# Kernel optimization log

Hardware: AMD Instinct MI355X
Metric: run time of the kernel (lower is better)

## Reference

```python
import jax, jax.numpy as jnp
import numpy as np

EPS = 1e-8  # torch F.cosine_similarity eps

B, H, K = 64, 2048, 256


def setup_inputs() -> dict:
    key = jax.random.key(0)
    k1, k2, k3, k4 = jax.random.split(key, 4)
    input_state = jax.random.normal(k1, (B, H), dtype=jnp.float32)
    knowledge_base = jax.random.normal(k2, (K, B, H), dtype=jnp.float32)
    W = jax.random.normal(k3, (H, H), dtype=jnp.float32) / np.sqrt(H)
    b = jax.random.normal(k4, (H,), dtype=jnp.float32) * 0.02
    return {"input_state": input_state, "knowledge_base": knowledge_base, "W": W, "b": b}


def reference(input_state, knowledge_base, W, b):
    # linear projection (torch Linear: x @ W.T + b)
    q = input_state @ W.T + b                      # [B, H]
    kproj = jnp.einsum('kbh,oh->kbo', knowledge_base, W) + b  # [K, B, H]
    # cosine similarity over last dim, with torch-style eps clamp on norms
    qn = jnp.maximum(jnp.linalg.norm(q, axis=-1), EPS)        # [B]
    kn = jnp.maximum(jnp.linalg.norm(kproj, axis=-1), EPS)    # [K, B]
    dots = jnp.einsum('bh,kbh->kb', q, kproj)                 # [K, B]
    scores = dots / (qn[None, :] * kn)                        # [K, B]
    # softmax over the K knowledge items
    attn = jax.nn.softmax(scores, axis=0)                     # [K, B]
    # output = input + softmax-weighted sum of (raw) knowledge items
    out = input_state + jnp.einsum('kb,kbh->bh', attn, knowledge_base)
    return out
```

## Files before the change

### kernel.cpp

```cpp
#include <hip/hip_runtime.h>
#include <hip/hip_bf16.h>

typedef unsigned short u16;
typedef unsigned int u32;
typedef unsigned long long u64;
typedef __attribute__((ext_vector_type(8))) short short8;
typedef __attribute__((ext_vector_type(4))) float float4v;

#define B_DIM 64
#define H_DIM 2048
#define K_DIM 256
#define NTHR  256

#define WS_WBF   0ull
#define WS_AQ    (8388608ull)
#define WS_Q     (WS_AQ + 524288ull)
#define WS_KN2   (WS_Q + 524288ull)
#define WS_DOTS  (WS_KN2 + 65536ull)
#define WS_KBF   (WS_DOTS + 65536ull)

__device__ __forceinline__ u16 f2bf(float f) {
    unsigned int u = __float_as_uint(f);
    unsigned int r = (u + 0x7fffu + ((u >> 16) & 1u)) >> 16;
    return (u16)r;
}

__device__ __forceinline__ u64 pack4(float4v v) {
    u64 a0 = f2bf(v.x), a1 = f2bf(v.y), a2 = f2bf(v.z), a3 = f2bf(v.w);
    return a0 | (a1 << 16) | (a2 << 32) | (a3 << 48);
}

__device__ __forceinline__ void llds16(const u16* g, u16* l) {
    __builtin_amdgcn_global_load_lds(
        (__attribute__((address_space(1))) void*)g,
        (__attribute__((address_space(3))) void*)l, 16, 0, 0);
}

__device__ __forceinline__ void gemm0_tile(const u16* __restrict__ Aq, const u16* __restrict__ Wb,
                                           float* __restrict__ qout, u16* As, u16* Bs,
                                           int nt, int ksplit) {
    const int tid = threadIdx.x;
    const int wave = tid >> 6, lane = tid & 63;
    const int l15 = lane & 15, qd = lane >> 4;
    const int wm = wave >> 1, wn = wave & 1;
    const int n0 = nt * 128;
    const int grow = lane >> 2;
    const int gcol = (((lane & 3) ^ ((lane >> 3) & 3)) * 8);
    const int sw = (l15 >> 1) & 3;
    float4v acc[4][4] = {};
    const int kb0 = ksplit * 512;
    for (int kk = 0; kk < 16; ++kk) {
        const int k0 = kb0 + kk * 32;
        #pragma unroll
        for (int i = 0; i < 2; ++i) {
            const int r = wave * 32 + i * 16;
            llds16(Wb + (size_t)(n0 + r + grow) * H_DIM + k0 + gcol, &Bs[r * 32]);
            llds16(Aq + (size_t)(r + grow) * H_DIM + k0 + gcol, &As[r * 32]);
        }
        __syncthreads();
        short8 af[4], bf_[4];
        #pragma unroll
        for (int mi = 0; mi < 4; ++mi)
            af[mi] = *(const short8*)&As[(wm * 64 + mi * 16 + l15) * 32 + ((qd ^ sw) * 8)];
        #pragma unroll
        for (int ni = 0; ni < 4; ++ni)
            bf_[ni] = *(const short8*)&Bs[(wn * 64 + ni * 16 + l15) * 32 + ((qd ^ sw) * 8)];
        #pragma unroll
        for (int mi = 0; mi < 4; ++mi)
            #pragma unroll
            for (int ni = 0; ni < 4; ++ni)
                acc[mi][ni] = __builtin_amdgcn_mfma_f32_16x16x32_bf16(af[mi], bf_[ni], acc[mi][ni], 0, 0, 0);
        __syncthreads();
    }
    const int n0w = n0 + wn * 64;
    if (wm == 0) {
        #pragma unroll
        for (int mi = 0; mi < 4; ++mi)
            #pragma unroll
            for (int reg = 0; reg < 4; ++reg) {
                const int m = mi * 16 + qd * 4 + reg;
                #pragma unroll
                for (int ni = 0; ni < 4; ++ni)
                    atomicAdd(&qout[m * H_DIM + n0w + ni * 16 + l15], acc[mi][ni][reg]);
            }
    }
}

__global__ __launch_bounds__(256) void prep_kernel(
        const float* __restrict__ W, const float* __restrict__ input,
        const float* __restrict__ bias, u16* __restrict__ Wb,
        u16* __restrict__ Aq, float* __restrict__ q,
        float* __restrict__ kn2, float* __restrict__ dots) {
    const int gid = blockIdx.x * NTHR + threadIdx.x;
    ((u64*)Wb)[gid] = pack4(((const float4v*)W)[gid]);
    if (gid < 65536) {
        u64 v = 0;
        if (gid < 32768) v = pack4(((const float4v*)input)[gid]);
        ((u64*)Aq)[gid] = v;
    }
    if (gid < 32768)
        ((float4v*)q)[gid] = ((const float4v*)bias)[gid & 511];
    if (gid < 4096) ((float4v*)kn2)[gid] = float4v{0.f, 0.f, 0.f, 0.f};
    else if (gid < 8192) ((float4v*)dots)[gid - 4096] = float4v{0.f, 0.f, 0.f, 0.f};
}

__global__ __launch_bounds__(256, 4) void mid_kernel(
        const float* __restrict__ kb, const u16* __restrict__ Aq,
        const u16* __restrict__ Wb, float* __restrict__ q, u16* __restrict__ Kbf) {
    __shared__ __align__(16) u16 As[128 * 32];
    __shared__ __align__(16) u16 Bs[128 * 32];
    const int bid = blockIdx.x;
    if (bid < 64) {
        gemm0_tile(Aq, Wb, q, As, Bs, bid & 15, bid >> 4);
    } else {
        const float4v* s4 = (const float4v*)kb;
        u64* d8 = (u64*)Kbf;
        for (int i = (bid - 64) * NTHR + threadIdx.x; i < 8388608; i += 960 * NTHR)
            d8[i] = pack4(s4[i]);
    }
}

__global__ __launch_bounds__(512, 2) void gemm_kernel(
        const u16* __restrict__ Kbf, const u16* __restrict__ Wb,
        const float* __restrict__ bias, const float* __restrict__ q,
        float* __restrict__ kn2, float* __restrict__ dots) {
    extern __shared__ __align__(16) u16 lds[];
    const int tid = threadIdx.x;
    const int wave = tid >> 6, lane = tid & 63;
    const int l15 = lane & 15, qd = lane >> 4;
    const int wm = wave >> 2, wn = wave & 3;
    const int nt = blockIdx.x & 7, mt = blockIdx.x >> 3;
    const int m0 = mt * 256, n0 = nt * 256;
    const int grow = wave * 16 + (lane >> 2);
    const int gcol = (((lane & 3) ^ ((lane >> 3) & 3)) * 8);
    const int sw = (l15 >> 1) & 3;

    const u16* srcA = Kbf + (size_t)(m0 + grow) * H_DIM + gcol;
    const u16* srcB = Wb + (size_t)(n0 + grow) * H_DIM + gcol;
    u16* dstBase = lds + wave * 512;

    auto stageA = [&](int t) {
        u16* d = dstBase + (t & 3) * 16384;
        const u16* s = srcA + t * 32;
        llds16(s, d);
        llds16(s + (size_t)128 * H_DIM, d + 4096);
    };
    auto stageB = [&](int t) {
        u16* d = dstBase + (t & 3) * 16384 + 8192;
        const u16* s = srcB + t * 32;
        llds16(s, d);
        llds16(s + (size_t)128 * H_DIM, d + 4096);
    };

    const int aoff = (wm * 128 + l15) * 32 + ((qd ^ sw) * 8);
    const int boff = (wn * 64 + l15) * 32 + ((qd ^ sw) * 8);

    float4v acc[8][4] = {};

    stageA(0); stageB(0); stageA(1); stageB(1); stageA(2); stageB(2);
    asm volatile("s_waitcnt vmcnt(8)" ::: "memory");
    __builtin_amdgcn_sched_barrier(0);
    __builtin_amdgcn_s_barrier();

    for (int t = 0; t < 64; ++t) {
        const u16* As = lds + (t & 3) * 16384;
        const u16* Bs = As + 8192;
        short8 af[4], bf_[4];
        #pragma unroll
        for (int ni = 0; ni < 4; ++ni)
            bf_[ni] = *(const short8*)&Bs[boff + ni * 512];
        #pragma unroll
        for (int mi = 0; mi < 4; ++mi)
            af[mi] = *(const short8*)&As[aoff + mi * 512];
        if (t + 3 < 64) stageA(t + 3);
        __builtin_amdgcn_s_barrier();
        asm volatile("s_waitcnt lgkmcnt(0)" ::: "memory");
        __builtin_amdgcn_sched_barrier(0);
        __builtin_amdgcn_s_setprio(1);
        #pragma unroll
        for (int mi = 0; mi < 4; ++mi)
            #pragma unroll
            for (int ni = 0; ni < 4; ++ni)
                acc[mi][ni] = __builtin_amdgcn_mfma_f32_16x16x32_bf16(af[mi], bf_[ni], acc[mi][ni], 0, 0, 0);
        __builtin_amdgcn_s_setprio(0);
        __builtin_amdgcn_s_barrier();
        #pragma unroll
        for (int mi = 0; mi < 4; ++mi)
            af[mi] = *(const short8*)&As[aoff + (4 + mi) * 512];
        if (t + 3 < 64) stageB(t + 3);
        __builtin_amdgcn_s_barrier();
        asm volatile("s_waitcnt lgkmcnt(0)" ::: "memory");
        __builtin_amdgcn_sched_barrier(0);
        __builtin_amdgcn_s_setprio(1);
        #pragma unroll
        for (int mi = 0; mi < 4; ++mi)
            #pragma unroll
            for (int ni = 0; ni < 4; ++ni)
                acc[4 + mi][ni] = __builtin_amdgcn_mfma_f32_16x16x32_bf16(af[mi], bf_[ni], acc[4 + mi][ni], 0, 0, 0);
        __builtin_amdgcn_s_setprio(0);
        if (t <= 60)      { asm volatile("s_waitcnt vmcnt(8)" ::: "memory"); }
        else if (t == 61) { asm volatile("s_waitcnt vmcnt(4)" ::: "memory"); }
        else if (t == 62) { asm volatile("s_waitcnt vmcnt(0)" ::: "memory"); }
        __builtin_amdgcn_sched_barrier(0);
        __builtin_amdgcn_s_barrier();
    }

    const int n0w = n0 + wn * 64;
    float bv[4];
    #pragma unroll
    for (int ni = 0; ni < 4; ++ni) bv[ni] = bias[n0w + ni * 16 + l15];
    #pragma unroll
    for (int mi = 0; mi < 8; ++mi)
        #pragma unroll
        for (int reg = 0; reg < 4; ++reg) {
            const int mloc = mi * 16 + qd * 4 + reg;
            const int mg = m0 + wm * 128 + mloc;
            const float* qrow = q + (mloc & 63) * H_DIM;
            float s2 = 0.f, sd = 0.f;
            #pragma unroll
            for (int ni = 0; ni < 4; ++ni) {
                const float y = acc[mi][ni][reg] + bv[ni];
                const float qv = qrow[n0w + ni * 16 + l15];
                s2 += y * y; sd += y * qv;
            }
            #pragma unroll
            for (int off = 1; off < 16; off <<= 1) {
                s2 += __shfl_xor(s2, off);
                sd += __shfl_xor(sd, off);
            }
            if (l15 == 0) {
                atomicAdd(&kn2[mg], s2);
                atomicAdd(&dots[mg], sd);
            }
        }
}

__global__ __launch_bounds__(256) void final_kernel(
        const float* __restrict__ input, const u16* __restrict__ Kbf,
        const float* __restrict__ q, const float* __restrict__ kn2,
        const float* __restrict__ dots, float* __restrict__ out) {
    __shared__ float sm[K_DIM];
    __shared__ float buf[4];
    const int b = blockIdx.x >> 2, hc = blockIdx.x & 3, tid = threadIdx.x;
    float s = 0.f;
    #pragma unroll
    for (int i = 0; i < 8; ++i) {
        float v = q[b * H_DIM + i * 256 + tid];
        s += v * v;
    }
    #pragma unroll
    for (int o = 32; o >= 1; o >>= 1) s += __shfl_xor(s, o);
    if ((tid & 63) == 0) buf[tid >> 6] = s;
    __syncthreads();
    const float qn = fmaxf(sqrtf(buf[0] + buf[1] + buf[2] + buf[3]), 1e-8f);
    __syncthreads();
    const float kn = fmaxf(sqrtf(kn2[tid * B_DIM + b]), 1e-8f);
    const float sc = dots[tid * B_DIM + b] / (qn * kn);
    float mx = sc;
    #pragma unroll
    for (int o = 32; o >= 1; o >>= 1) mx = fmaxf(mx, __shfl_xor(mx, o));
    if ((tid & 63) == 0) buf[tid >> 6] = mx;
    __syncthreads();
    mx = fmaxf(fmaxf(buf[0], buf[1]), fmaxf(buf[2], buf[3]));
    __syncthreads();
    const float e = expf(sc - mx);
    float se = e;
    #pragma unroll
    for (int o = 32; o >= 1; o >>= 1) se += __shfl_xor(se, o);
    if ((tid & 63) == 0) buf[tid >> 6] = se;
    __syncthreads();
    se = buf[0] + buf[1] + buf[2] + buf[3];
    sm[tid] = e / se;
    __syncthreads();
    const u32* base = (const u32*)Kbf;
    const int h2 = hc * 256 + tid;
    float s0 = 0.f, s1 = 0.f;
    #pragma unroll 8
    for (int k = 0; k < K_DIM; ++k) {
        const u32 p = base[(size_t)(k * B_DIM + b) * (H_DIM / 2) + h2];
        const float a = sm[k];
        s0 += a * __uint_as_float(p << 16);
        s1 += a * __uint_as_float(p & 0xffff0000u);
    }
    const int h = h2 * 2;
    float2 iv = *(const float2*)&input[(size_t)b * H_DIM + h];
    float2 r; r.x = iv.x + s0; r.y = iv.y + s1;
    *(float2*)&out[(size_t)b * H_DIM + h] = r;
}

extern "C" void kernel_launch(void* const* d_in, const int* in_sizes, int n_in,
                              void* d_out, int out_size, void* d_ws, size_t ws_size,
                              hipStream_t stream) {
    const float* input = (const float*)d_in[0];
    const float* kb    = (const float*)d_in[1];
    const float* W     = (const float*)d_in[2];
    const float* bias  = (const float*)d_in[3];
    float* out = (float*)d_out;
    char* ws = (char*)d_ws;

    u16*   Wb   = (u16*)(ws + WS_WBF);
    u16*   Aq   = (u16*)(ws + WS_AQ);
    float* q    = (float*)(ws + WS_Q);
    float* kn2  = (float*)(ws + WS_KN2);
    float* dots = (float*)(ws + WS_DOTS);
    u16*   Kbf  = (u16*)(ws + WS_KBF);

    static int lds_set = 0;
    if (!lds_set) {
        hipFuncSetAttribute((const void*)gemm_kernel,
                            hipFuncAttributeMaxDynamicSharedMemorySize, 131072);
        lds_set = 1;
    }

    prep_kernel<<<4096, NTHR, 0, stream>>>(W, input, bias, Wb, Aq, q, kn2, dots);
    mid_kernel<<<1024, NTHR, 0, stream>>>(kb, Aq, Wb, q, Kbf);
    gemm_kernel<<<512, 512, 131072, stream>>>(Kbf, Wb, bias, q, kn2, dots);
    final_kernel<<<256, NTHR, 0, stream>>>(input, Kbf, q, kn2, dots, out);
}
```

Baseline: 380.3 us.

## Restructure GEMM main loop with register double-buffering and move KB conversion to prep

The main GEMM loop is rewritten as a two-step unrolled macro that prefetches the next tile's A/B fragments from LDS into a second register set while the current MFMAs run. This removes one barrier per half-step and relaxes the vmcnt waits. The fp32-to-bf16 conversion of the knowledge base moves from mid_kernel into prep_kernel. The small q GEMM is split across 16 K-chunks instead of 4, so it runs on 256 blocks. The aim is to hide LDS latency and raise GEMM occupancy, at the cost of more registers and a change to when cross-wave synchronisation happens.

```diff
diff --git a/kernel.cpp b/kernel.cpp
--- a/kernel.cpp
+++ b/kernel.cpp
@@ -48,8 +48,8 @@
     const int gcol = (((lane & 3) ^ ((lane >> 3) & 3)) * 8);
     const int sw = (l15 >> 1) & 3;
     float4v acc[4][4] = {};
-    const int kb0 = ksplit * 512;
-    for (int kk = 0; kk < 16; ++kk) {
+    const int kb0 = ksplit * 128;
+    for (int kk = 0; kk < 4; ++kk) {
         const int k0 = kb0 + kk * 32;
         #pragma unroll
         for (int i = 0; i < 2; ++i) {
@@ -87,12 +87,20 @@
 }
 
 __global__ __launch_bounds__(256) void prep_kernel(
-        const float* __restrict__ W, const float* __restrict__ input,
-        const float* __restrict__ bias, u16* __restrict__ Wb,
+        const float* __restrict__ W, const float* __restrict__ kb,
+        const float* __restrict__ input, const float* __restrict__ bias,
+        u16* __restrict__ Wb, u16* __restrict__ Kbf,
         u16* __restrict__ Aq, float* __restrict__ q,
         float* __restrict__ kn2, float* __restrict__ dots) {
     const int gid = blockIdx.x * NTHR + threadIdx.x;
     ((u64*)Wb)[gid] = pack4(((const float4v*)W)[gid]);
+    {
+        const float4v* s4 = (const float4v*)kb;
+        u64* d8 = (u64*)Kbf;
+        #pragma unroll
+        for (int i = 0; i < 8; ++i)
+            d8[gid + i * 1048576] = pack4(s4[gid + i * 1048576]);
+    }
     if (gid < 65536) {
         u64 v = 0;
         if (gid < 32768) v = pack4(((const float4v*)input)[gid]);
@@ -105,20 +113,50 @@
 }
 
 __global__ __launch_bounds__(256, 4) void mid_kernel(
-        const float* __restrict__ kb, const u16* __restrict__ Aq,
-        const u16* __restrict__ Wb, float* __restrict__ q, u16* __restrict__ Kbf) {
+        const u16* __restrict__ Aq, const u16* __restrict__ Wb, float* __restrict__ q) {
     __shared__ __align__(16) u16 As[128 * 32];
     __shared__ __align__(16) u16 Bs[128 * 32];
-    const int bid = blockIdx.x;
-    if (bid < 64) {
-        gemm0_tile(Aq, Wb, q, As, Bs, bid & 15, bid >> 4);
-    } else {
-        const float4v* s4 = (const float4v*)kb;
-        u64* d8 = (u64*)Kbf;
-        for (int i = (bid - 64) * NTHR + threadIdx.x; i < 8388608; i += 960 * NTHR)
-            d8[i] = pack4(s4[i]);
-    }
-}
+    gemm0_tile(Aq, Wb, q, As, Bs, blockIdx.x & 15, blockIdx.x >> 4);
+}
+
+#define TILE_BODY(T, bfC, a0C, bfN, a0N)                                        \
+  {                                                                             \
+    const int t_ = (T);                                                         \
+    const u16* As_ = lds + (t_ & 3) * 16384;                                    \
+    const u16* Bs_ = As_ + 8192;                                                \
+    if (t_ + 3 < 64) stageA(t_ + 3);                                            \
+    asm volatile("s_waitcnt lgkmcnt(0)" ::: "memory");                          \
+    __builtin_amdgcn_sched_barrier(0);                                          \
+    __builtin_amdgcn_s_setprio(1);                                              \
+    _Pragma("unroll") for (int mi = 0; mi < 4; ++mi)                            \
+      _Pragma("unroll") for (int ni = 0; ni < 4; ++ni)                          \
+        acc[mi][ni] = __builtin_amdgcn_mfma_f32_16x16x32_bf16(a0C[mi], bfC[ni], acc[mi][ni], 0, 0, 0); \
+    __builtin_amdgcn_s_setprio(0);                                              \
+    __builtin_amdgcn_sched_barrier(0);                                          \
+    _Pragma("unroll") for (int mi = 0; mi < 4; ++mi)                            \
+        a0C[mi] = *(const short8*)&As_[aoff + (4 + mi) * 512];                  \
+    if (t_ + 1 < 64) {                                                          \
+      const u16* Asn_ = lds + ((t_ + 1) & 3) * 16384;                           \
+      const u16* Bsn_ = Asn_ + 8192;                                            \
+      _Pragma("unroll") for (int ni = 0; ni < 4; ++ni)                          \
+          bfN[ni] = *(const short8*)&Bsn_[boff + ni * 512];                     \
+      _Pragma("unroll") for (int mi = 0; mi < 4; ++mi)                          \
+          a0N[mi] = *(const short8*)&Asn_[aoff + mi * 512];                     \
+    }                                                                           \
+    if (t_ + 3 < 64) stageB(t_ + 3);                                            \
+    if (t_ + 1 < 64) { asm volatile("s_waitcnt lgkmcnt(8)" ::: "memory"); }     \
+    else             { asm volatile("s_waitcnt lgkmcnt(0)" ::: "memory"); }     \
+    __builtin_amdgcn_sched_barrier(0);                                          \
+    __builtin_amdgcn_s_setprio(1);                                              \
+    _Pragma("unroll") for (int mi = 0; mi < 4; ++mi)                            \
+      _Pragma("unroll") for (int ni = 0; ni < 4; ++ni)                          \
+        acc[4 + mi][ni] = __builtin_amdgcn_mfma_f32_16x16x32_bf16(a0C[mi], bfC[ni], acc[4 + mi][ni], 0, 0, 0); \
+    __builtin_amdgcn_s_setprio(0);                                              \
+    __builtin_amdgcn_sched_barrier(0);                                          \
+    if (t_ <= 60) { asm volatile("s_waitcnt vmcnt(4)" ::: "memory"); }          \
+    else          { asm volatile("s_waitcnt vmcnt(0)" ::: "memory"); }          \
+    __builtin_amdgcn_s_barrier();                                               \
+  }
 
 __global__ __launch_bounds__(512, 2) void gemm_kernel(
         const u16* __restrict__ Kbf, const u16* __restrict__ Wb,
@@ -156,53 +194,24 @@
     const int boff = (wn * 64 + l15) * 32 + ((qd ^ sw) * 8);
 
     float4v acc[8][4] = {};
+    short8 bf0[4], a00[4], bf1[4], a01[4];
 
     stageA(0); stageB(0); stageA(1); stageB(1); stageA(2); stageB(2);
-    asm volatile("s_waitcnt vmcnt(8)" ::: "memory");
+    asm volatile("s_waitcnt vmcnt(4)" ::: "memory");
     __builtin_amdgcn_sched_barrier(0);
     __builtin_amdgcn_s_barrier();
-
-    for (int t = 0; t < 64; ++t) {
-        const u16* As = lds + (t & 3) * 16384;
-        const u16* Bs = As + 8192;
-        short8 af[4], bf_[4];
-        #pragma unroll
-        for (int ni = 0; ni < 4; ++ni)
-            bf_[ni] = *(const short8*)&Bs[boff + ni * 512];
-        #pragma unroll
-        for (int mi = 0; mi < 4; ++mi)
-            af[mi] = *(const short8*)&As[aoff + mi * 512];
-        if (t + 3 < 64) stageA(t + 3);
-        __builtin_amdgcn_s_barrier();
-        asm volatile("s_waitcnt lgkmcnt(0)" ::: "memory");
-        __builtin_amdgcn_sched_barrier(0);
-        __builtin_amdgcn_s_setprio(1);
-        #pragma unroll
-        for (int mi = 0; mi < 4; ++mi)
-            #pragma unroll
-            for (int ni = 0; ni < 4; ++ni)
-                acc[mi][ni] = __builtin_amdgcn_mfma_f32_16x16x32_bf16(af[mi], bf_[ni], acc[mi][ni], 0, 0, 0);
-        __builtin_amdgcn_s_setprio(0);
-        __builtin_amdgcn_s_barrier();
-        #pragma unroll
-        for (int mi = 0; mi < 4; ++mi)
-            af[mi] = *(const short8*)&As[aoff + (4 + mi) * 512];
-        if (t + 3 < 64) stageB(t + 3);
-        __builtin_amdgcn_s_barrier();
-        asm volatile("s_waitcnt lgkmcnt(0)" ::: "memory");
-        __builtin_amdgcn_sched_barrier(0);
-        __builtin_amdgcn_s_setprio(1);
-        #pragma unroll
-        for (int mi = 0; mi < 4; ++mi)
-            #pragma unroll
-            for (int ni = 0; ni < 4; ++ni)
-                acc[4 + mi][ni] = __builtin_amdgcn_mfma_f32_16x16x32_bf16(af[mi], bf_[ni], acc[4 + mi][ni], 0, 0, 0);
-        __builtin_amdgcn_s_setprio(0);
-        if (t <= 60)      { asm volatile("s_waitcnt vmcnt(8)" ::: "memory"); }
-        else if (t == 61) { asm volatile("s_waitcnt vmcnt(4)" ::: "memory"); }
-        else if (t == 62) { asm volatile("s_waitcnt vmcnt(0)" ::: "memory"); }
-        __builtin_amdgcn_sched_barrier(0);
-        __builtin_amdgcn_s_barrier();
+    {
+        const u16* As0 = lds;
+        const u16* Bs0 = lds + 8192;
+        #pragma unroll
+        for (int ni = 0; ni < 4; ++ni) bf0[ni] = *(const short8*)&Bs0[boff + ni * 512];
+        #pragma unroll
+        for (int mi = 0; mi < 4; ++mi) a00[mi] = *(const short8*)&As0[aoff + mi * 512];
+    }
+
+    for (int t = 0; t < 64; t += 2) {
+        TILE_BODY(t,     bf0, a00, bf1, a01);
+        TILE_BODY(t + 1, bf1, a01, bf0, a00);
     }
 
     const int n0w = n0 + wn * 64;
@@ -312,8 +321,8 @@
         lds_set = 1;
     }
 
-    prep_kernel<<<4096, NTHR, 0, stream>>>(W, input, bias, Wb, Aq, q, kn2, dots);
-    mid_kernel<<<1024, NTHR, 0, stream>>>(kb, Aq, Wb, q, Kbf);
+    prep_kernel<<<4096, NTHR, 0, stream>>>(W, kb, input, bias, Wb, Kbf, Aq, q, kn2, dots);
+    mid_kernel<<<256, NTHR, 0, stream>>>(Aq, Wb, q);
     gemm_kernel<<<512, 512, 131072, stream>>>(Kbf, Wb, bias, q, kn2, dots);
     final_kernel<<<256, NTHR, 0, stream>>>(input, Kbf, q, kn2, dots, out);
 }
```

Result: slower. 391.6 us (+3.0%).

## Switch GEMM main loop to 64-wide K tiles with double buffering

Applied to the files above, without the earlier changes.

The main projection GEMM loop moves from a 4-stage ring of 32-wide K slices to a 2-stage double buffer of 64-wide K slices. Each iteration now issues four MFMA phases with a new 8-way XOR swizzle on 128-byte LDS rows. This halves loop iterations and stage bookkeeping. In exchange, prefetch depth drops to one tile ahead and every iteration ends with a full vmcnt(0) wait, which can expose global load latency.

```diff
diff --git a/kernel.cpp b/kernel.cpp
--- a/kernel.cpp
+++ b/kernel.cpp
@@ -30,7 +30,7 @@
     return a0 | (a1 << 16) | (a2 << 32) | (a3 << 48);
 }
 
-__device__ __forceinline__ void llds16(const u16* g, u16* l) {
+__device__ __forceinline__ void llds16(const u16* g, const u16* l) {
     __builtin_amdgcn_global_load_lds(
         (__attribute__((address_space(1))) void*)g,
         (__attribute__((address_space(3))) void*)l, 16, 0, 0);
@@ -127,52 +127,53 @@
     extern __shared__ __align__(16) u16 lds[];
     const int tid = threadIdx.x;
     const int wave = tid >> 6, lane = tid & 63;
-    const int l15 = lane & 15, qd = lane >> 4;
+    const int l15 = lane & 15, qd = (lane >> 4) & 3;
     const int wm = wave >> 2, wn = wave & 3;
     const int nt = blockIdx.x & 7, mt = blockIdx.x >> 3;
     const int m0 = mt * 256, n0 = nt * 256;
-    const int grow = wave * 16 + (lane >> 2);
-    const int gcol = (((lane & 3) ^ ((lane >> 3) & 3)) * 8);
-    const int sw = (l15 >> 1) & 3;
-
-    const u16* srcA = Kbf + (size_t)(m0 + grow) * H_DIM + gcol;
-    const u16* srcB = Wb + (size_t)(n0 + grow) * H_DIM + gcol;
-    u16* dstBase = lds + wave * 512;
-
-    auto stageA = [&](int t) {
-        u16* d = dstBase + (t & 3) * 16384;
-        const u16* s = srcA + t * 32;
-        llds16(s, d);
-        llds16(s + (size_t)128 * H_DIM, d + 4096);
-    };
-    auto stageB = [&](int t) {
-        u16* d = dstBase + (t & 3) * 16384 + 8192;
-        const u16* s = srcB + t * 32;
-        llds16(s, d);
-        llds16(s + (size_t)128 * H_DIM, d + 4096);
-    };
-
-    const int aoff = (wm * 128 + l15) * 32 + ((qd ^ sw) * 8);
-    const int boff = (wn * 64 + l15) * 32 + ((qd ^ sw) * 8);
+
+    const int srow = wave * 8 + (lane >> 3);
+    const int gsrc = (lane & 7) ^ ((lane >> 3) & 7);
+    const u16* sA = Kbf + (size_t)(m0 + srow) * H_DIM + gsrc * 8;
+    const u16* sB = Wb  + (size_t)(n0 + srow) * H_DIM + gsrc * 8;
+    const int dst0 = wave * 512;
+
+    const int sx = lane & 7;
+    const int kq0 = (qd ^ sx) * 8;
+    const int kq1 = ((4 + qd) ^ sx) * 8;
+    const int aBase = wm * 8192 + l15 * 64;
+    const int bBase = 16384 + (wn >> 1) * 8192 + ((wn & 1) * 64 + l15) * 64;
 
     float4v acc[8][4] = {};
-
-    stageA(0); stageB(0); stageA(1); stageB(1); stageA(2); stageB(2);
-    asm volatile("s_waitcnt vmcnt(8)" ::: "memory");
+    short8 aP[4], aQ[4], bP[4], bQ[4];
+
+    llds16(sA,                          lds + dst0);
+    llds16(sA + (size_t) 64 * H_DIM,    lds + 4096  + dst0);
+    llds16(sA + (size_t)128 * H_DIM,    lds + 8192  + dst0);
+    llds16(sA + (size_t)192 * H_DIM,    lds + 12288 + dst0);
+    llds16(sB,                          lds + 16384 + dst0);
+    llds16(sB + (size_t) 64 * H_DIM,    lds + 20480 + dst0);
+    llds16(sB + (size_t)128 * H_DIM,    lds + 24576 + dst0);
+    llds16(sB + (size_t)192 * H_DIM,    lds + 28672 + dst0);
+    asm volatile("s_waitcnt vmcnt(0)" ::: "memory");
     __builtin_amdgcn_sched_barrier(0);
     __builtin_amdgcn_s_barrier();
 
-    for (int t = 0; t < 64; ++t) {
-        const u16* As = lds + (t & 3) * 16384;
-        const u16* Bs = As + 8192;
-        short8 af[4], bf_[4];
-        #pragma unroll
-        for (int ni = 0; ni < 4; ++ni)
-            bf_[ni] = *(const short8*)&Bs[boff + ni * 512];
-        #pragma unroll
-        for (int mi = 0; mi < 4; ++mi)
-            af[mi] = *(const short8*)&As[aoff + mi * 512];
-        if (t + 3 < 64) stageA(t + 3);
+    for (int it = 0; it < 32; ++it) {
+        const u16* cur = lds + (it & 1) * 32768;
+        const u16* nxt = lds + ((it + 1) & 1) * 32768;
+        const bool st = (it < 31);
+        const size_t c1 = (size_t)(it + 1) * 64;
+        #pragma unroll
+        for (int ni = 0; ni < 4; ++ni) bP[ni] = *(const short8*)&cur[bBase + ni * 1024 + kq0];
+        #pragma unroll
+        for (int mi = 0; mi < 4; ++mi) aP[mi] = *(const short8*)&cur[aBase + mi * 1024 + kq0];
+        if (st) {
+            llds16(sA + c1,                         nxt + dst0);
+            llds16(sA + (size_t) 64 * H_DIM + c1,   nxt + 4096  + dst0);
+            llds16(sA + (size_t)128 * H_DIM + c1,   nxt + 8192  + dst0);
+            llds16(sA + (size_t)192 * H_DIM + c1,   nxt + 12288 + dst0);
+        }
         __builtin_amdgcn_s_barrier();
         asm volatile("s_waitcnt lgkmcnt(0)" ::: "memory");
         __builtin_amdgcn_sched_barrier(0);
@@ -181,13 +182,17 @@
         for (int mi = 0; mi < 4; ++mi)
             #pragma unroll
             for (int ni = 0; ni < 4; ++ni)
-                acc[mi][ni] = __builtin_amdgcn_mfma_f32_16x16x32_bf16(af[mi], bf_[ni], acc[mi][ni], 0, 0, 0);
+                acc[mi][ni] = __builtin_amdgcn_mfma_f32_16x16x32_bf16(aP[mi], bP[ni], acc[mi][ni], 0, 0, 0);
         __builtin_amdgcn_s_setprio(0);
         __builtin_amdgcn_s_barrier();
         #pragma unroll
-        for (int mi = 0; mi < 4; ++mi)
-            af[mi] = *(const short8*)&As[aoff + (4 + mi) * 512];
-        if (t + 3 < 64) stageB(t + 3);
+        for (int mi = 0; mi < 4; ++mi) aQ[mi] = *(const short8*)&cur[aBase + (4 + mi) * 1024 + kq0];
+        if (st) {
+            llds16(sB + c1,                         nxt + 16384 + dst0);
+            llds16(sB + (size_t) 64 * H_DIM + c1,   nxt + 20480 + dst0);
+            llds16(sB + (size_t)128 * H_DIM + c1,   nxt + 24576 + dst0);
+            llds16(sB + (size_t)192 * H_DIM + c1,   nxt + 28672 + dst0);
+        }
         __builtin_amdgcn_s_barrier();
         asm volatile("s_waitcnt lgkmcnt(0)" ::: "memory");
         __builtin_amdgcn_sched_barrier(0);
@@ -196,11 +201,37 @@
         for (int mi = 0; mi < 4; ++mi)
             #pragma unroll
             for (int ni = 0; ni < 4; ++ni)
-                acc[4 + mi][ni] = __builtin_amdgcn_mfma_f32_16x16x32_bf16(af[mi], bf_[ni], acc[4 + mi][ni], 0, 0, 0);
+                acc[4 + mi][ni] = __builtin_amdgcn_mfma_f32_16x16x32_bf16(aQ[mi], bP[ni], acc[4 + mi][ni], 0, 0, 0);
         __builtin_amdgcn_s_setprio(0);
-        if (t <= 60)      { asm volatile("s_waitcnt vmcnt(8)" ::: "memory"); }
-        else if (t == 61) { asm volatile("s_waitcnt vmcnt(4)" ::: "memory"); }
-        else if (t == 62) { asm volatile("s_waitcnt vmcnt(0)" ::: "memory"); }
+        __builtin_amdgcn_s_barrier();
+        #pragma unroll
+        for (int ni = 0; ni < 4; ++ni) bQ[ni] = *(const short8*)&cur[bBase + ni * 1024 + kq1];
+        #pragma unroll
+        for (int mi = 0; mi < 4; ++mi) aP[mi] = *(const short8*)&cur[aBase + mi * 1024 + kq1];
+        __builtin_amdgcn_s_barrier();
+        asm volatile("s_waitcnt lgkmcnt(0)" ::: "memory");
+        __builtin_amdgcn_sched_barrier(0);
+        __builtin_amdgcn_s_setprio(1);
+        #pragma unroll
+        for (int mi = 0; mi < 4; ++mi)
+            #pragma unroll
+            for (int ni = 0; ni < 4; ++ni)
+                acc[mi][ni] = __builtin_amdgcn_mfma_f32_16x16x32_bf16(aP[mi], bQ[ni], acc[mi][ni], 0, 0, 0);
+        __builtin_amdgcn_s_setprio(0);
+        __builtin_amdgcn_s_barrier();
+        #pragma unroll
+        for (int mi = 0; mi < 4; ++mi) aQ[mi] = *(const short8*)&cur[aBase + (4 + mi) * 1024 + kq1];
+        __builtin_amdgcn_s_barrier();
+        asm volatile("s_waitcnt lgkmcnt(0)" ::: "memory");
+        __builtin_amdgcn_sched_barrier(0);
+        __builtin_amdgcn_s_setprio(1);
+        #pragma unroll
+        for (int mi = 0; mi < 4; ++mi)
+            #pragma unroll
+            for (int ni = 0; ni < 4; ++ni)
+                acc[4 + mi][ni] = __builtin_amdgcn_mfma_f32_16x16x32_bf16(aQ[mi], bQ[ni], acc[4 + mi][ni], 0, 0, 0);
+        __builtin_amdgcn_s_setprio(0);
+        asm volatile("s_waitcnt vmcnt(0)" ::: "memory");
         __builtin_amdgcn_sched_barrier(0);
         __builtin_amdgcn_s_barrier();
     }
```

After: 372.5 us. -2.0%, faster.
